# Kernel tuning notes

Hardware: AMD Instinct MI355X
Metric: run time of the kernel (lower is better)

## Reference

```python
import jax, jax.numpy as jnp
import numpy as np

L = 32            # num_layers
R = 16            # lora_rank
P = L * 7         # 224 projections
D = 256           # encoder d_model
H = 4             # encoder heads
HD = D // H
FF = 2048         # TransformerEncoderLayer default dim_feedforward
PED = 512         # proj_embed_dim
HID = 4096
KV = 8 * (4096 // 32)   # 1024
INTER = 11008
VOCAB = 50000
NEG = -1e9

# projection index groups within the P=7*L ordering [q,k,v,o,gate,up,down]
IDX_A_HID = jnp.asarray((np.arange(L)[:, None] * 7 + np.array([0, 1, 2, 3, 4, 5])).reshape(-1))  # in_dim=4096
IDX_A_INT = jnp.asarray(np.arange(L) * 7 + 6)                                                    # in_dim=11008
IDX_B_HID = jnp.asarray((np.arange(L)[:, None] * 7 + np.array([0, 3, 6])).reshape(-1))           # out_dim=4096
IDX_B_KV  = jnp.asarray((np.arange(L)[:, None] * 7 + np.array([1, 2])).reshape(-1))              # out_dim=1024
IDX_B_INT = jnp.asarray((np.arange(L)[:, None] * 7 + np.array([4, 5])).reshape(-1))              # out_dim=11008


def _ln(x, g, b, eps=1e-5):
    m = jnp.mean(x, -1, keepdims=True)
    v = jnp.mean((x - m) ** 2, -1, keepdims=True)
    return (x - m) * jax.lax.rsqrt(v + eps) * g + b


def _enc_layer(x, pad, qw, qb, ow, ob, g1, b1, f1w, f1b, f2w, f2b, g2, b2):
    # post-norm TransformerEncoderLayer (torch default), relu FFN, eval mode (no dropout)
    Bsz, S, _ = x.shape
    qkv = x @ qw.T + qb                                  # [B,S,3D]
    q, k, v = jnp.split(qkv, 3, axis=-1)
    hd = lambda t: t.reshape(Bsz, S, H, HD).transpose(0, 2, 1, 3)
    q, k, v = hd(q), hd(k), hd(v)
    s = jnp.einsum('bhqd,bhkd->bhqk', q, k) / jnp.asarray(np.sqrt(HD), x.dtype)
    s = jnp.where(pad[:, None, None, :], NEG, s)
    a = jax.nn.softmax(s, -1)
    o = jnp.einsum('bhqk,bhkd->bhqd', a, v).transpose(0, 2, 1, 3).reshape(Bsz, S, D)
    x = _ln(x + o @ ow.T + ob, g1, b1)
    f = jax.nn.relu(x @ f1w.T + f1b) @ f2w.T + f2b
    return _ln(x + f, g2, b2)


def _forward(condition_ids, attention_mask, embed_table, enc_qkv_w, enc_qkv_b, enc_out_w, enc_out_b,
             enc_ln1_g, enc_ln1_b, enc_ff1_w, enc_ff1_b, enc_ff2_w, enc_ff2_b, enc_ln2_g, enc_ln2_b,
             proj_w, proj_b, a1_w, a1_b, a2_w, a2_b, b1_w, b1_b, b2_w, b2_b, scales):
    Bsz = condition_ids.shape[0]
    x = embed_table[condition_ids]                       # [B,S,256]
    pad = attention_mask == 0                            # key padding mask (~attention_mask)
    for l in range(3):
        x = _enc_layer(x, pad, enc_qkv_w[l], enc_qkv_b[l], enc_out_w[l], enc_out_b[l],
                       enc_ln1_g[l], enc_ln1_b[l], enc_ff1_w[l], enc_ff1_b[l],
                       enc_ff2_w[l], enc_ff2_b[l], enc_ln2_g[l], enc_ln2_b[l])
    am = attention_mask.astype(x.dtype)
    pooled = (x * am[..., None]).sum(1) / jnp.clip(am.sum(1, keepdims=True), 1.0)   # masked mean pool
    pe = (pooled @ proj_w.T + proj_b).reshape(Bsz, P, PED)                          # [B,224,512]

    def dec(w1, b1_, w2, b2_):
        return jax.nn.gelu(pe @ w1.T + b1_, approximate=False) @ w2.T + b2_

    A_base = dec(a1_w, a1_b, a2_w, a2_b).reshape(Bsz, P, R, 64)   # [B,P,r,64]
    B_base = dec(b1_w, b1_b, b2_w, b2_b).reshape(Bsz, P, 64, R)   # [B,P,64,r]
    sa, sb = scales[:, 0], scales[:, 1]

    def tile_A(idx, in_d):
        # all in_dims divisible by 64 => repeat(in_d//64+1)[:, :in_d] == exact tiling
        a = A_base[:, idx] * sa[idx][None, :, None, None]
        return jnp.tile(a, (1, 1, 1, in_d // 64))

    def tile_B(idx, out_d):
        b = B_base[:, idx] * sb[idx][None, :, None, None]
        return jnp.tile(b, (1, 1, out_d // 64, 1))

    return (tile_A(IDX_A_HID, HID), tile_A(IDX_A_INT, INTER),
            tile_B(IDX_B_HID, HID), tile_B(IDX_B_KV, KV), tile_B(IDX_B_INT, INTER))


def setup_inputs() -> dict:
    key = jax.random.key(0)
    ks = iter(jax.random.split(key, 40))
    rn = lambda shape, s=0.02: jax.random.normal(next(ks), shape, jnp.float32) * s
    Bsz, S = 4, 128
    return {
        'condition_ids': jax.random.randint(next(ks), (Bsz, S), 0, VOCAB),
        'attention_mask': jnp.ones((Bsz, S), jnp.int32),
        'embed_table': rn((VOCAB, D)),
        'enc_qkv_w': rn((3, 3 * D, D)), 'enc_qkv_b': rn((3, 3 * D)),
        'enc_out_w': rn((3, D, D)), 'enc_out_b': rn((3, D)),
        'enc_ln1_g': jnp.ones((3, D)), 'enc_ln1_b': jnp.zeros((3, D)),
        'enc_ff1_w': rn((3, FF, D)), 'enc_ff1_b': rn((3, FF)),
        'enc_ff2_w': rn((3, D, FF)), 'enc_ff2_b': rn((3, D)),
        'enc_ln2_g': jnp.ones((3, D)), 'enc_ln2_b': jnp.zeros((3, D)),
        'proj_w': rn((P * PED, D)), 'proj_b': rn((P * PED,)),
        'a1_w': rn((D, PED)), 'a1_b': rn((D,)),
        'a2_w': rn((R * 64, D)), 'a2_b': rn((R * 64,)),
        'b1_w': rn((D, PED)), 'b1_b': rn((D,)),
        'b2_w': rn((R * 64, D)), 'b2_b': rn((R * 64,)),
        'scales': jnp.full((P, 2), 0.01, jnp.float32),
    }


def reference(condition_ids, attention_mask, embed_table, enc_qkv_w, enc_qkv_b, enc_out_w, enc_out_b,
              enc_ln1_g, enc_ln1_b, enc_ff1_w, enc_ff1_b, enc_ff2_w, enc_ff2_b, enc_ln2_g, enc_ln2_b,
              proj_w, proj_b, a1_w, a1_b, a2_w, a2_b, b1_w, b1_b, b2_w, b2_b, scales):
    return _forward(condition_ids, attention_mask, embed_table, enc_qkv_w, enc_qkv_b, enc_out_w, enc_out_b,
                    enc_ln1_g, enc_ln1_b, enc_ff1_w, enc_ff1_b, enc_ff2_w, enc_ff2_b, enc_ln2_g, enc_ln2_b,
                    proj_w, proj_b, a1_w, a1_b, a2_w, a2_b, b1_w, b1_b, b2_w, b2_b, scales)
```

## Files before the change

kernel.cpp:

```cpp
#include <hip/hip_runtime.h>
#include <hip/hip_bf16.h>

typedef unsigned short u16;
typedef unsigned int u32;
typedef __attribute__((ext_vector_type(8))) short short8;
typedef __attribute__((ext_vector_type(4))) float floatx4;

__device__ __forceinline__ u16 f2bf(float f) {
  u32 x = __float_as_uint(f);
  x += 0x7FFFu + ((x >> 16) & 1u);
  return (u16)(x >> 16);
}
__device__ __forceinline__ u32 pk2(float lo, float hi) {
  return (u32)f2bf(lo) | ((u32)f2bf(hi) << 16);
}

__global__ void embed_kernel(const int* __restrict__ ids, const float* __restrict__ emb,
                             float* __restrict__ x) {
  int tok = blockIdx.x, d = threadIdx.x;
  x[tok * 256 + d] = emb[(size_t)ids[tok] * 256 + d];
}

template <int ACT, int SPLIT>
__global__ __launch_bounds__(256) void mfma_gemm_kernel(
    const float* __restrict__ A, int lda,
    const float* __restrict__ Wa, const float* __restrict__ Wb, int nsplit, int koffb,
    const float* __restrict__ biasa, const float* __restrict__ biasb,
    float* __restrict__ Ca, float* __restrict__ Cb,
    int N, int K, int KS, int pstride) {
  __shared__ u16 Abf[2][64 * 32];
  __shared__ u16 Wbf[2][64 * 32];
  const int t = threadIdx.x;
  const int m0 = blockIdx.x * 64;
  int n0 = blockIdx.y * 64;
  const int kz = blockIdx.z;
  const float* W = Wa;
  const float* bias = biasa;
  const float* Ain = A;
  float* C = Ca;
  if (n0 >= nsplit) { n0 -= nsplit; W = Wb; bias = biasb; C = Cb; Ain = A + koffb; }
  const int srow = t >> 2, skc = (t & 3) * 8;
  const int w = t >> 6, lane = t & 63;
  const int q = lane >> 4, rr = lane & 15;
  floatx4 acc[4];
#pragma unroll
  for (int i = 0; i < 4; ++i) acc[i] = (floatx4){0.f, 0.f, 0.f, 0.f};

  const int kbeg = kz * KS, kend = kbeg + KS;
  const float* ga = Ain + (size_t)(m0 + srow) * lda + kbeg + skc;
  const float* gw = W + (size_t)(n0 + srow) * K + kbeg + skc;
  float4 a0 = *(const float4*)ga;
  float4 a1 = *(const float4*)(ga + 4);
  float4 w0 = *(const float4*)gw;
  float4 w1 = *(const float4*)(gw + 4);
  int buf = 0;
  for (int k0 = kbeg; k0 < kend; k0 += 32) {
    uint4 pa, pw;
    pa.x = pk2(a0.x, a0.y); pa.y = pk2(a0.z, a0.w);
    pa.z = pk2(a1.x, a1.y); pa.w = pk2(a1.z, a1.w);
    pw.x = pk2(w0.x, w0.y); pw.y = pk2(w0.z, w0.w);
    pw.z = pk2(w1.x, w1.y); pw.w = pk2(w1.z, w1.w);
    *(uint4*)&Abf[buf][t * 8] = pa;
    *(uint4*)&Wbf[buf][t * 8] = pw;
    if (k0 + 32 < kend) {
      ga += 32; gw += 32;
      a0 = *(const float4*)ga;
      a1 = *(const float4*)(ga + 4);
      w0 = *(const float4*)gw;
      w1 = *(const float4*)(gw + 4);
    }
    __syncthreads();
    short8 af = *(short8*)&Abf[buf][(w * 16 + rr) * 32 + q * 8];
#pragma unroll
    for (int ct = 0; ct < 4; ++ct) {
      short8 bfv = *(short8*)&Wbf[buf][(ct * 16 + rr) * 32 + q * 8];
      acc[ct] = __builtin_amdgcn_mfma_f32_16x16x32_bf16(af, bfv, acc[ct], 0, 0, 0);
    }
    buf ^= 1;
  }

  float* dst = SPLIT ? (C + (size_t)kz * pstride) : C;
#pragma unroll
  for (int ct = 0; ct < 4; ++ct) {
    int col = n0 + ct * 16 + rr;
#pragma unroll
    for (int r = 0; r < 4; ++r) {
      int row = m0 + w * 16 + q * 4 + r;
      float v = acc[ct][r];
      if (!SPLIT) {
        v += bias[col];
        if (ACT == 1) v = fmaxf(v, 0.f);
        if (ACT == 2) v = 0.5f * v * (1.f + erff(v * 0.70710678118654752f));
      }
      dst[(size_t)row * N + col] = v;
    }
  }
}

__global__ __launch_bounds__(256) void red_gelu_dual_kernel(const float* __restrict__ pa,
    const float* __restrict__ pb, const float* __restrict__ ba, const float* __restrict__ bb,
    float* __restrict__ h) {
  int blk = blockIdx.x;
  int second = blk >= 896;
  int row = second ? blk - 896 : blk;
  const float* parts = second ? pb : pa;
  const float* bias = second ? bb : ba;
  int c = threadIdx.x;
  float v = bias[c];
#pragma unroll
  for (int p = 0; p < 4; ++p) v += parts[(size_t)p * 229376 + row * 256 + c];
  v = 0.5f * v * (1.f + erff(v * 0.70710678118654752f));
  h[(size_t)row * 512 + second * 256 + c] = v;
}

__global__ __launch_bounds__(256) void attn_kernel(const float* __restrict__ qkv,
    const int* __restrict__ mask, float* __restrict__ o) {
  __shared__ float Klds[8192];
  const int blk = blockIdx.x;
  const int b = blk >> 7, h = (blk >> 5) & 3, qg = blk & 31;
  const int t = threadIdx.x;
  for (int i = t; i < 8192; i += 256) {
    int s = i >> 6, d = i & 63;
    Klds[(s << 6) + (d ^ (s & 31))] = qkv[(size_t)(b * 128 + s) * 768 + h * 64 + 256 + d];
  }
  __syncthreads();
  const int wave = t >> 6, lane = t & 63;
  const int q = qg * 4 + wave;
  float qv = qkv[(size_t)(b * 128 + q) * 768 + h * 64 + lane];
  const int m0i = mask[b * 128 + lane];
  const int m1i = mask[b * 128 + 64 + lane];
  float s0 = 0.f, s1 = 0.f;
  const int sw = lane & 31;
  for (int d = 0; d < 64; ++d) {
    float qd = __shfl(qv, d);
    s0 += qd * Klds[(lane << 6) + (d ^ sw)];
    s1 += qd * Klds[((lane + 64) << 6) + (d ^ sw)];
  }
  s0 *= 0.125f; s1 *= 0.125f;
  if (m0i == 0) s0 = -1000000000.0f;
  if (m1i == 0) s1 = -1000000000.0f;
  float m = fmaxf(s0, s1);
  for (int off = 32; off; off >>= 1) m = fmaxf(m, __shfl_xor(m, off));
  float p0 = expf(s0 - m), p1 = expf(s1 - m);
  float sum = p0 + p1;
  for (int off = 32; off; off >>= 1) sum += __shfl_xor(sum, off);
  float rs = 1.f / sum;
  const float* vb = qkv + (size_t)b * 98304 + h * 64 + 512 + lane;
  float acc = 0.f;
#pragma unroll
  for (int k = 0; k < 64; ++k) acc += __shfl(p0, k) * vb[(size_t)k * 768];
#pragma unroll
  for (int k = 0; k < 64; ++k) acc += __shfl(p1, k) * vb[(size_t)(k + 64) * 768];
  o[(size_t)(b * 128 + q) * 256 + h * 64 + lane] = acc * rs;
}

__global__ __launch_bounds__(256) void add_ln_red_kernel(float* __restrict__ x,
    const float* __restrict__ parts, int nparts, int pstride, const float* __restrict__ bias,
    const float* __restrict__ g, const float* __restrict__ b) {
  int tok = blockIdx.x, t = threadIdx.x;
  int idx = tok * 256 + t;
  float r = x[idx] + bias[t];
  for (int p = 0; p < nparts; ++p) r += parts[(size_t)p * pstride + idx];
  float s = r, sq = r * r;
  for (int off = 32; off; off >>= 1) { s += __shfl_xor(s, off); sq += __shfl_xor(sq, off); }
  __shared__ float red[8];
  int wave = t >> 6, lane = t & 63;
  if (lane == 0) { red[wave] = s; red[4 + wave] = sq; }
  __syncthreads();
  float S = red[0] + red[1] + red[2] + red[3];
  float SQ = red[4] + red[5] + red[6] + red[7];
  float mean = S * (1.f / 256.f);
  float var = SQ * (1.f / 256.f) - mean * mean;
  float inv = 1.f / sqrtf(fmaxf(var, 0.f) + 1e-5f);
  x[idx] = (r - mean) * inv * g[t] + b[t];
}

__global__ void pool_kernel(const float* __restrict__ x, const int* __restrict__ mask,
                            float* __restrict__ pooled) {
  int b = blockIdx.x, d = threadIdx.x;
  float s = 0.f, c = 0.f;
  for (int ss = 0; ss < 128; ++ss) {
    float m = (float)mask[b * 128 + ss];
    s += m * x[(size_t)(b * 128 + ss) * 256 + d];
    c += m;
  }
  pooled[b * 256 + d] = s / fmaxf(c, 1.f);
}

__global__ __launch_bounds__(256) void proj_kernel(const float* __restrict__ pooled,
    const float* __restrict__ W, const float* __restrict__ bias, float* __restrict__ pe) {
  __shared__ float pl[1024];
  int t = threadIdx.x;
  for (int i = t; i < 1024; i += 256) pl[i] = pooled[i];
  __syncthreads();
  int wave = t >> 6, lane = t & 63;
  int half = lane >> 5, sl = lane & 31;
  int row = blockIdx.x * 8 + wave * 2 + half;
  float4 w0 = *(const float4*)(W + (size_t)row * 256 + sl * 8);
  float4 w1 = *(const float4*)(W + (size_t)row * 256 + sl * 8 + 4);
  float a0, a1, a2, a3;
#pragma unroll
  for (int bb = 0; bb < 4; ++bb) {
    const float* pp = &pl[bb * 256 + sl * 8];
    float v = w0.x * pp[0] + w0.y * pp[1] + w0.z * pp[2] + w0.w * pp[3]
            + w1.x * pp[4] + w1.y * pp[5] + w1.z * pp[6] + w1.w * pp[7];
    if (bb == 0) a0 = v; else if (bb == 1) a1 = v; else if (bb == 2) a2 = v; else a3 = v;
  }
#pragma unroll
  for (int off = 1; off < 32; off <<= 1) {
    a0 += __shfl_xor(a0, off); a1 += __shfl_xor(a1, off);
    a2 += __shfl_xor(a2, off); a3 += __shfl_xor(a3, off);
  }
  if (sl == 0) {
    float bv = bias[row];
    pe[0 * 114688 + row] = a0 + bv;
    pe[1 * 114688 + row] = a1 + bv;
    pe[2 * 114688 + row] = a2 + bv;
    pe[3 * 114688 + row] = a3 + bv;
  }
}

__global__ __launch_bounds__(256) void tile_a_kernel(const float* __restrict__ Abase,
    const float* __restrict__ scales, float* __restrict__ out, int nI, int ind,
    int pdiv, int pmul, int padd) {
  int row = blockIdx.x;
  int r = row & 15, bi = row >> 4;
  int i = bi % nI, b = bi / nI;
  int p = (i / pdiv) * 7 + (i % pdiv) * pmul + padd;
  float s = scales[2 * p];
  __shared__ float chunk[64];
  int t = threadIdx.x;
  if (t < 64) chunk[t] = Abase[((size_t)(b * 224 + p) * 16 + r) * 64 + t] * s;
  __syncthreads();
  size_t ob = (size_t)row * ind;
  for (int u = t; u * 4 < ind; u += 256) {
    int c0 = u * 4;
    float4 ov = *(const float4*)&chunk[c0 & 63];
    *(float4*)(out + ob + c0) = ov;
  }
}

__global__ __launch_bounds__(256) void tile_b_kernel(const float* __restrict__ Bbase,
    const float* __restrict__ scales, float* __restrict__ out, int nI, int ind, int nchunks,
    int pdiv, int pmul, int padd) {
  int blk = blockIdx.x;
  int cc = blk % nchunks, bi = blk / nchunks;
  int i = bi % nI, b = bi / nI;
  int p = (i / pdiv) * 7 + (i % pdiv) * pmul + padd;
  float s = scales[2 * p + 1];
  __shared__ float chunk[1024];
  int t = threadIdx.x;
  for (int e = t; e < 1024; e += 256) chunk[e] = Bbase[(size_t)(b * 224 + p) * 1024 + e] * s;
  __syncthreads();
  int cchunk16 = (ind / nchunks) * 16;
  size_t ob = (size_t)bi * ind * 16 + (size_t)cc * cchunk16;
  for (int u = t; u * 4 < cchunk16; u += 256) {
    int e0 = u * 4;
    int cabs = (cc * cchunk16 + e0) >> 4;
    int src = ((cabs & 63) << 4) + (e0 & 15);
    float4 ov = *(const float4*)&chunk[src];
    *(float4*)(out + ob + e0) = ov;
  }
}

extern "C" void kernel_launch(void* const* d_in, const int* in_sizes, int n_in,
                              void* d_out, int out_size, void* d_ws, size_t ws_size,
                              hipStream_t stream) {
  const int* ids     = (const int*)d_in[0];
  const int* mask    = (const int*)d_in[1];
  const float* emb   = (const float*)d_in[2];
  const float* qkv_w = (const float*)d_in[3];
  const float* qkv_b = (const float*)d_in[4];
  const float* out_w = (const float*)d_in[5];
  const float* out_b = (const float*)d_in[6];
  const float* ln1_g = (const float*)d_in[7];
  const float* ln1_b = (const float*)d_in[8];
  const float* ff1_w = (const float*)d_in[9];
  const float* ff1_b = (const float*)d_in[10];
  const float* ff2_w = (const float*)d_in[11];
  const float* ff2_b = (const float*)d_in[12];
  const float* ln2_g = (const float*)d_in[13];
  const float* ln2_b = (const float*)d_in[14];
  const float* proj_w = (const float*)d_in[15];
  const float* proj_b = (const float*)d_in[16];
  const float* a1_w = (const float*)d_in[17];
  const float* a1_b = (const float*)d_in[18];
  const float* a2_w = (const float*)d_in[19];
  const float* a2_b = (const float*)d_in[20];
  const float* b1_w = (const float*)d_in[21];
  const float* b1_b = (const float*)d_in[22];
  const float* b2_w = (const float*)d_in[23];
  const float* b2_b = (const float*)d_in[24];
  const float* scales = (const float*)d_in[25];

  float* w = (float*)d_ws;
  float* x      = w + 0;
  float* qkv    = w + 262144;
  float* attn_o = w + 655360;
  float* ff     = w + 786432;
  float* pooled = w + 1835008;
  float* pe     = w + 1836032;
  float* hbuf   = w + 2294784;
  float* Abase  = w + 2753536;
  float* Bbase  = w + 3671040;
  float* parts  = w + 4588544;

  float* out = (float*)d_out;
  const int NSB = 1 << 30;

  embed_kernel<<<512, 256, 0, stream>>>(ids, emb, x);
  for (int l = 0; l < 3; ++l) {
    mfma_gemm_kernel<0, 0><<<dim3(8, 12), 256, 0, stream>>>(
        x, 256, qkv_w + l * 768 * 256, nullptr, NSB, 0, qkv_b + l * 768, nullptr,
        qkv, nullptr, 768, 256, 256, 0);
    attn_kernel<<<512, 256, 0, stream>>>(qkv, mask, attn_o);
    mfma_gemm_kernel<0, 1><<<dim3(8, 4, 4), 256, 0, stream>>>(
        attn_o, 256, out_w + l * 256 * 256, nullptr, NSB, 0, nullptr, nullptr,
        parts, nullptr, 256, 256, 64, 131072);
    add_ln_red_kernel<<<512, 256, 0, stream>>>(x, parts, 4, 131072, out_b + l * 256,
                                               ln1_g + l * 256, ln1_b + l * 256);
    mfma_gemm_kernel<1, 0><<<dim3(8, 32), 256, 0, stream>>>(
        x, 256, ff1_w + l * 2048 * 256, nullptr, NSB, 0, ff1_b + l * 2048, nullptr,
        ff, nullptr, 2048, 256, 256, 0);
    mfma_gemm_kernel<0, 1><<<dim3(8, 4, 8), 256, 0, stream>>>(
        ff, 2048, ff2_w + l * 256 * 2048, nullptr, NSB, 0, nullptr, nullptr,
        parts, nullptr, 256, 2048, 256, 131072);
    add_ln_red_kernel<<<512, 256, 0, stream>>>(x, parts, 8, 131072, ff2_b + l * 256,
                                               ln2_g + l * 256, ln2_b + l * 256);
  }
  pool_kernel<<<4, 256, 0, stream>>>(x, mask, pooled);
  proj_kernel<<<14336, 256, 0, stream>>>(pooled, proj_w, proj_b, pe);

  mfma_gemm_kernel<0, 1><<<dim3(14, 8, 4), 256, 0, stream>>>(
      pe, 512, a1_w, b1_w, 256, 0, nullptr, nullptr,
      parts, ff, 256, 512, 128, 229376);
  red_gelu_dual_kernel<<<1792, 256, 0, stream>>>(parts, ff, a1_b, b1_b, hbuf);
  mfma_gemm_kernel<0, 0><<<dim3(14, 32), 256, 0, stream>>>(
      hbuf, 512, a2_w, b2_w, 1024, 256, a2_b, b2_b,
      Abase, Bbase, 1024, 256, 256, 0);

  tile_a_kernel<<<12288, 256, 0, stream>>>(Abase, scales, out, 192, 4096, 6, 1, 0);
  tile_a_kernel<<<2048, 256, 0, stream>>>(Abase, scales, out + 50331648ull, 32, 11008, 1, 0, 6);
  tile_b_kernel<<<3072, 256, 0, stream>>>(Bbase, scales, out + 72876032ull, 96, 4096, 8, 3, 3, 0);
  tile_b_kernel<<<512, 256, 0, stream>>>(Bbase, scales, out + 98041856ull, 64, 1024, 2, 2, 1, 1);
  tile_b_kernel<<<2048, 256, 0, stream>>>(Bbase, scales, out + 102236160ull, 64, 11008, 8, 2, 1, 4);
}
```

Before: 921.7 us.

## Widen GEMM K-chunk with swizzled LDS, drop out-proj split-K, fuse tile kernels

The MFMA GEMM now stages 128-wide K chunks in a single XOR-swizzled LDS buffer, doing four MFMA steps per barrier instead of one. This cuts the number of syncs and avoids LDS bank conflicts. The encoder out-projection no longer uses split-K: it writes the biased result directly, and the add+LN kernel just sums one part. The five output tiling launches become a single kernel that branches on block index, saving launch overhead. In exchange, register pressure goes up because 16 float4 values are held per thread, and global-load prefetch now overlaps less with compute.

```diff
diff --git a/kernel.cpp b/kernel.cpp
--- a/kernel.cpp
+++ b/kernel.cpp
@@ -28,8 +28,10 @@
     const float* __restrict__ biasa, const float* __restrict__ biasb,
     float* __restrict__ Ca, float* __restrict__ Cb,
     int N, int K, int KS, int pstride) {
-  __shared__ u16 Abf[2][64 * 32];
-  __shared__ u16 Wbf[2][64 * 32];
+  constexpr int CHUNK = 128;
+  constexpr int NF4 = CHUNK / 16;
+  __shared__ u16 Abf[64 * CHUNK];
+  __shared__ u16 Wbf[64 * CHUNK];
   const int t = threadIdx.x;
   const int m0 = blockIdx.x * 64;
   int n0 = blockIdx.y * 64;
@@ -39,9 +41,12 @@
   const float* Ain = A;
   float* C = Ca;
   if (n0 >= nsplit) { n0 -= nsplit; W = Wb; bias = biasb; C = Cb; Ain = A + koffb; }
-  const int srow = t >> 2, skc = (t & 3) * 8;
+  const int srow = t >> 2, skc = (t & 3) * (CHUNK / 4);
+  const int sr7 = srow & 7;
+  const int g0 = skc >> 3;
   const int w = t >> 6, lane = t & 63;
   const int q = lane >> 4, rr = lane & 15;
+  const int r7 = rr & 7;
   floatx4 acc[4];
 #pragma unroll
   for (int i = 0; i < 4; ++i) acc[i] = (floatx4){0.f, 0.f, 0.f, 0.f};
@@ -49,34 +54,44 @@
   const int kbeg = kz * KS, kend = kbeg + KS;
   const float* ga = Ain + (size_t)(m0 + srow) * lda + kbeg + skc;
   const float* gw = W + (size_t)(n0 + srow) * K + kbeg + skc;
-  float4 a0 = *(const float4*)ga;
-  float4 a1 = *(const float4*)(ga + 4);
-  float4 w0 = *(const float4*)gw;
-  float4 w1 = *(const float4*)(gw + 4);
-  int buf = 0;
-  for (int k0 = kbeg; k0 < kend; k0 += 32) {
-    uint4 pa, pw;
-    pa.x = pk2(a0.x, a0.y); pa.y = pk2(a0.z, a0.w);
-    pa.z = pk2(a1.x, a1.y); pa.w = pk2(a1.z, a1.w);
-    pw.x = pk2(w0.x, w0.y); pw.y = pk2(w0.z, w0.w);
-    pw.z = pk2(w1.x, w1.y); pw.w = pk2(w1.z, w1.w);
-    *(uint4*)&Abf[buf][t * 8] = pa;
-    *(uint4*)&Wbf[buf][t * 8] = pw;
-    if (k0 + 32 < kend) {
-      ga += 32; gw += 32;
-      a0 = *(const float4*)ga;
-      a1 = *(const float4*)(ga + 4);
-      w0 = *(const float4*)gw;
-      w1 = *(const float4*)(gw + 4);
+  float4 ar[NF4], wr[NF4];
+#pragma unroll
+  for (int j = 0; j < NF4; ++j) {
+    ar[j] = *(const float4*)(ga + 4 * j);
+    wr[j] = *(const float4*)(gw + 4 * j);
+  }
+  for (int kc = kbeg; kc < kend; kc += CHUNK) {
+    if (kc != kbeg) __syncthreads();
+#pragma unroll
+    for (int j = 0; j < NF4 / 2; ++j) {
+      uint4 pa, pw;
+      pa.x = pk2(ar[2 * j].x, ar[2 * j].y);     pa.y = pk2(ar[2 * j].z, ar[2 * j].w);
+      pa.z = pk2(ar[2 * j + 1].x, ar[2 * j + 1].y); pa.w = pk2(ar[2 * j + 1].z, ar[2 * j + 1].w);
+      pw.x = pk2(wr[2 * j].x, wr[2 * j].y);     pw.y = pk2(wr[2 * j].z, wr[2 * j].w);
+      pw.z = pk2(wr[2 * j + 1].x, wr[2 * j + 1].y); pw.w = pk2(wr[2 * j + 1].z, wr[2 * j + 1].w);
+      int gs = (g0 + j) ^ sr7;
+      *(uint4*)&Abf[srow * CHUNK + (gs << 3)] = pa;
+      *(uint4*)&Wbf[srow * CHUNK + (gs << 3)] = pw;
+    }
+    if (kc + CHUNK < kend) {
+      ga += CHUNK; gw += CHUNK;
+#pragma unroll
+      for (int j = 0; j < NF4; ++j) {
+        ar[j] = *(const float4*)(ga + 4 * j);
+        wr[j] = *(const float4*)(gw + 4 * j);
+      }
     }
     __syncthreads();
-    short8 af = *(short8*)&Abf[buf][(w * 16 + rr) * 32 + q * 8];
-#pragma unroll
-    for (int ct = 0; ct < 4; ++ct) {
-      short8 bfv = *(short8*)&Wbf[buf][(ct * 16 + rr) * 32 + q * 8];
-      acc[ct] = __builtin_amdgcn_mfma_f32_16x16x32_bf16(af, bfv, acc[ct], 0, 0, 0);
+#pragma unroll
+    for (int ks = 0; ks < CHUNK / 32; ++ks) {
+      int gA = ks * 4 + q;
+      short8 af = *(short8*)&Abf[(w * 16 + rr) * CHUNK + (((gA ^ r7)) << 3)];
+#pragma unroll
+      for (int ct = 0; ct < 4; ++ct) {
+        short8 bfv = *(short8*)&Wbf[(ct * 16 + rr) * CHUNK + (((gA ^ r7)) << 3)];
+        acc[ct] = __builtin_amdgcn_mfma_f32_16x16x32_bf16(af, bfv, acc[ct], 0, 0, 0);
+      }
     }
-    buf ^= 1;
   }
 
   float* dst = SPLIT ? (C + (size_t)kz * pstride) : C;
@@ -159,7 +174,7 @@
     const float* __restrict__ g, const float* __restrict__ b) {
   int tok = blockIdx.x, t = threadIdx.x;
   int idx = tok * 256 + t;
-  float r = x[idx] + bias[t];
+  float r = x[idx] + (bias ? bias[t] : 0.f);
   for (int p = 0; p < nparts; ++p) r += parts[(size_t)p * pstride + idx];
   float s = r, sq = r * r;
   for (int off = 32; off; off >>= 1) { s += __shfl_xor(s, off); sq += __shfl_xor(sq, off); }
@@ -220,16 +235,13 @@
   }
 }
 
-__global__ __launch_bounds__(256) void tile_a_kernel(const float* __restrict__ Abase,
+__device__ __forceinline__ void tile_a_body(const float* __restrict__ Abase,
     const float* __restrict__ scales, float* __restrict__ out, int nI, int ind,
-    int pdiv, int pmul, int padd) {
-  int row = blockIdx.x;
+    int pdiv, int pmul, int padd, int row, int t, float* chunk) {
   int r = row & 15, bi = row >> 4;
   int i = bi % nI, b = bi / nI;
   int p = (i / pdiv) * 7 + (i % pdiv) * pmul + padd;
   float s = scales[2 * p];
-  __shared__ float chunk[64];
-  int t = threadIdx.x;
   if (t < 64) chunk[t] = Abase[((size_t)(b * 224 + p) * 16 + r) * 64 + t] * s;
   __syncthreads();
   size_t ob = (size_t)row * ind;
@@ -240,16 +252,13 @@
   }
 }
 
-__global__ __launch_bounds__(256) void tile_b_kernel(const float* __restrict__ Bbase,
+__device__ __forceinline__ void tile_b_body(const float* __restrict__ Bbase,
     const float* __restrict__ scales, float* __restrict__ out, int nI, int ind, int nchunks,
-    int pdiv, int pmul, int padd) {
-  int blk = blockIdx.x;
+    int pdiv, int pmul, int padd, int blk, int t, float* chunk) {
   int cc = blk % nchunks, bi = blk / nchunks;
   int i = bi % nI, b = bi / nI;
   int p = (i / pdiv) * 7 + (i % pdiv) * pmul + padd;
   float s = scales[2 * p + 1];
-  __shared__ float chunk[1024];
-  int t = threadIdx.x;
   for (int e = t; e < 1024; e += 256) chunk[e] = Bbase[(size_t)(b * 224 + p) * 1024 + e] * s;
   __syncthreads();
   int cchunk16 = (ind / nchunks) * 16;
@@ -260,6 +269,24 @@
     int src = ((cabs & 63) << 4) + (e0 & 15);
     float4 ov = *(const float4*)&chunk[src];
     *(float4*)(out + ob + e0) = ov;
+  }
+}
+
+__global__ __launch_bounds__(256) void tile_all_kernel(const float* __restrict__ Abase,
+    const float* __restrict__ Bbase, const float* __restrict__ scales,
+    float* __restrict__ out) {
+  __shared__ float chunk[1024];
+  int blk = blockIdx.x, t = threadIdx.x;
+  if (blk < 12288) {
+    tile_a_body(Abase, scales, out, 192, 4096, 6, 1, 0, blk, t, chunk);
+  } else if (blk < 14336) {
+    tile_a_body(Abase, scales, out + 50331648ull, 32, 11008, 1, 0, 6, blk - 12288, t, chunk);
+  } else if (blk < 17408) {
+    tile_b_body(Bbase, scales, out + 72876032ull, 96, 4096, 8, 3, 3, 0, blk - 14336, t, chunk);
+  } else if (blk < 17920) {
+    tile_b_body(Bbase, scales, out + 98041856ull, 64, 1024, 2, 2, 1, 1, blk - 17408, t, chunk);
+  } else {
+    tile_b_body(Bbase, scales, out + 102236160ull, 64, 11008, 8, 2, 1, 4, blk - 17920, t, chunk);
   }
 }
 
@@ -314,10 +341,10 @@
         x, 256, qkv_w + l * 768 * 256, nullptr, NSB, 0, qkv_b + l * 768, nullptr,
         qkv, nullptr, 768, 256, 256, 0);
     attn_kernel<<<512, 256, 0, stream>>>(qkv, mask, attn_o);
-    mfma_gemm_kernel<0, 1><<<dim3(8, 4, 4), 256, 0, stream>>>(
-        attn_o, 256, out_w + l * 256 * 256, nullptr, NSB, 0, nullptr, nullptr,
-        parts, nullptr, 256, 256, 64, 131072);
-    add_ln_red_kernel<<<512, 256, 0, stream>>>(x, parts, 4, 131072, out_b + l * 256,
+    mfma_gemm_kernel<0, 0><<<dim3(8, 4), 256, 0, stream>>>(
+        attn_o, 256, out_w + l * 256 * 256, nullptr, NSB, 0, out_b + l * 256, nullptr,
+        parts, nullptr, 256, 256, 256, 0);
+    add_ln_red_kernel<<<512, 256, 0, stream>>>(x, parts, 1, 0, nullptr,
                                                ln1_g + l * 256, ln1_b + l * 256);
     mfma_gemm_kernel<1, 0><<<dim3(8, 32), 256, 0, stream>>>(
         x, 256, ff1_w + l * 2048 * 256, nullptr, NSB, 0, ff1_b + l * 2048, nullptr,
@@ -339,9 +366,5 @@
       hbuf, 512, a2_w, b2_w, 1024, 256, a2_b, b2_b,
       Abase, Bbase, 1024, 256, 256, 0);
 
-  tile_a_kernel<<<12288, 256, 0, stream>>>(Abase, scales, out, 192, 4096, 6, 1, 0);
-  tile_a_kernel<<<2048, 256, 0, stream>>>(Abase, scales, out + 50331648ull, 32, 11008, 1, 0, 6);
-  tile_b_kernel<<<3072, 256, 0, stream>>>(Bbase, scales, out + 72876032ull, 96, 4096, 8, 3, 3, 0);
-  tile_b_kernel<<<512, 256, 0, stream>>>(Bbase, scales, out + 98041856ull, 64, 1024, 2, 2, 1, 1);
-  tile_b_kernel<<<2048, 256, 0, stream>>>(Bbase, scales, out + 102236160ull, 64, 11008, 8, 2, 1, 4);
-}
+  tile_all_kernel<<<19968, 256, 0, stream>>>(Abase, Bbase, scales, out);
+}
```

Measured after the change: 916.2 us. Within noise of the previous version (-0.6%).
